# Performance work log

Measured on AMD Instinct MI355X. Metric: run time of the kernel, lower is better.

## Reference

```python
import jax, jax.numpy as jnp
import numpy as np

N_NODES = 100000
N_EDGES = 600000
IN_C, HID_C, OUT_C = 128, 128, 64


def gcn_conv(x, W, b, src, dst, n_nodes):
    """PyG GCNConv: out = D^{-1/2} (A + I) D^{-1/2} X W + b (symmetric norm, self-loops)."""
    h = x @ W  # [N, C_out] transform first (as PyG does)
    # add self loops
    loop = jnp.arange(n_nodes, dtype=src.dtype)
    s = jnp.concatenate([src, loop])
    d = jnp.concatenate([dst, loop])
    # degree over targets (edge weight = 1)
    deg = jax.ops.segment_sum(jnp.ones_like(d, dtype=h.dtype), d, num_segments=n_nodes)
    dinv = jnp.where(deg > 0, jax.lax.rsqrt(deg), 0.0)
    norm = dinv[s] * dinv[d]  # [E+N]
    msg = h[s] * norm[:, None]  # gather + scale
    out = jax.ops.segment_sum(msg, d, num_segments=n_nodes)  # scatter-add
    return out + b


def setup_inputs() -> dict:
    key = jax.random.key(0)
    k1, k2, k3, k4, k5 = jax.random.split(key, 5)
    x = jax.random.normal(k1, (N_NODES, IN_C), dtype=jnp.float32)
    src = jax.random.randint(k2, (N_EDGES,), 0, N_NODES, dtype=jnp.int32)
    dst = jax.random.randint(k3, (N_EDGES,), 0, N_NODES, dtype=jnp.int32)
    # Glorot-style init for conv weights, zero bias (PyG defaults)
    W1 = jax.random.normal(k4, (IN_C, HID_C), dtype=jnp.float32) * (1.0 / np.sqrt(IN_C))
    W2 = jax.random.normal(k5, (HID_C, OUT_C), dtype=jnp.float32) * (1.0 / np.sqrt(HID_C))
    b1 = jnp.zeros((HID_C,), dtype=jnp.float32)
    b2 = jnp.zeros((OUT_C,), dtype=jnp.float32)
    return {"x": x, "W1": W1, "b1": b1, "W2": W2, "b2": b2, "src": src, "dst": dst}


def reference(x, W1, b1, W2, b2, src, dst):
    h = gcn_conv(x, W1, b1, src, dst, N_NODES)
    h = jax.nn.relu(h)
    out = gcn_conv(h, W2, b2, src, dst, N_NODES)
    return out
```

## Files before the change

### kernel.cpp

```cpp
#include <hip/hip_runtime.h>
#include <math.h>


typedef __bf16 bf16x8 __attribute__((ext_vector_type(8)));
typedef float f32x4 __attribute__((ext_vector_type(4)));

union ABu {
  unsigned short u16[8];
  uint4 u4;
  bf16x8 v;
};

__device__ inline unsigned short f2bf(float f) {
  unsigned u = __float_as_uint(f);
  return (unsigned short)((u + 0x7fffu + ((u >> 16) & 1u)) >> 16);
}

__device__ inline void unpack8(uint4 v, float* f) {
  f[0] = __uint_as_float(v.x << 16);
  f[1] = __uint_as_float(v.x & 0xffff0000u);
  f[2] = __uint_as_float(v.y << 16);
  f[3] = __uint_as_float(v.y & 0xffff0000u);
  f[4] = __uint_as_float(v.z << 16);
  f[5] = __uint_as_float(v.z & 0xffff0000u);
  f[6] = __uint_as_float(v.w << 16);
  f[7] = __uint_as_float(v.w & 0xffff0000u);
}

__device__ inline uint4 pack8(const float* a) {
  uint4 o;
  o.x = (unsigned)f2bf(a[0]) | ((unsigned)f2bf(a[1]) << 16);
  o.y = (unsigned)f2bf(a[2]) | ((unsigned)f2bf(a[3]) << 16);
  o.z = (unsigned)f2bf(a[4]) | ((unsigned)f2bf(a[5]) << 16);
  o.w = (unsigned)f2bf(a[6]) | ((unsigned)f2bf(a[7]) << 16);
  return o;
}

constexpr int SCAN_CHUNK = 1024;

__global__ __launch_bounds__(256) void k_pre(const float* __restrict__ W1,
                                             const float* __restrict__ W2,
                                             unsigned short* __restrict__ Wb1,
                                             unsigned short* __restrict__ Wb2,
                                             int* __restrict__ counts, int n) {
  constexpr int CONV_BLOCKS = (128 * 128 + 128 * 64) / 256;
  if (blockIdx.x < CONV_BLOCKS) {
    int idx = blockIdx.x * 256 + threadIdx.x;
    if (idx < 128 * 128) {
      int k = idx >> 7, c = idx & 127;
      Wb1[(((k >> 3) << 7) + c) * 8 + (k & 7)] = f2bf(W1[idx]);
    } else {
      int j = idx - 128 * 128;
      int k = j >> 6, c = j & 63;
      Wb2[(((k >> 3) << 6) + c) * 8 + (k & 7)] = f2bf(W2[j]);
    }
    return;
  }
  int i = (blockIdx.x - CONV_BLOCKS) * 256 + threadIdx.x;
  if (i < n) counts[i] = 0;
}

__global__ __launch_bounds__(256) void k_gemm1(const float* __restrict__ X,
                                               const unsigned short* __restrict__ Wb,
                                               unsigned short* __restrict__ Cb, int M) {
  constexpr int K = 128, N = 128, NT = N / 16, KS = K / 32;
  const int tid = threadIdx.x;
  const int wave = tid >> 6;
  const int lane = tid & 63;
  const int q = lane >> 4;
  const int l15 = lane & 15;
  const int row0 = blockIdx.x * 64 + wave * 16;
  const int rowA = row0 + l15;

  f32x4 zero = {0.0f, 0.0f, 0.0f, 0.0f};
  f32x4 acc[NT];
#pragma unroll
  for (int t = 0; t < NT; ++t) acc[t] = zero;

#pragma unroll
  for (int kk = 0; kk < KS; ++kk) {
    ABu a;
    float4 f0 = make_float4(0.f, 0.f, 0.f, 0.f);
    float4 f1 = make_float4(0.f, 0.f, 0.f, 0.f);
    if (rowA < M) {
      const float4* ap = (const float4*)(X + (size_t)rowA * K + kk * 32 + q * 8);
      f0 = ap[0];
      f1 = ap[1];
    }
    a.u16[0] = f2bf(f0.x); a.u16[1] = f2bf(f0.y);
    a.u16[2] = f2bf(f0.z); a.u16[3] = f2bf(f0.w);
    a.u16[4] = f2bf(f1.x); a.u16[5] = f2bf(f1.y);
    a.u16[6] = f2bf(f1.z); a.u16[7] = f2bf(f1.w);
#pragma unroll
    for (int nt = 0; nt < NT; ++nt) {
      ABu b;
      b.u4 = *(const uint4*)(Wb + ((size_t)(kk * 4 + q) * N + nt * 16 + l15) * 8);
      acc[nt] = __builtin_amdgcn_mfma_f32_16x16x32_bf16(a.v, b.v, acc[nt], 0, 0, 0);
    }
  }

#pragma unroll
  for (int v = 0; v < 4; ++v) {
    int row = row0 + q * 4 + v;
    if (row < M) {
#pragma unroll
      for (int nt = 0; nt < NT; ++nt)
        Cb[(size_t)row * N + nt * 16 + l15] = f2bf(acc[nt][v]);
    }
  }
}

__global__ void k_count_rank(const int* __restrict__ dst, int* __restrict__ counts,
                             int* __restrict__ rank, int E) {
  int e = blockIdx.x * blockDim.x + threadIdx.x;
  if (e < E) rank[e] = atomicAdd(&counts[dst[e]], 1);
}

__global__ __launch_bounds__(256) void k_scan1(const int* __restrict__ counts,
                                               int* __restrict__ offsets,
                                               int* __restrict__ aux, int n) {
  __shared__ int tsum[256];
  int tid = threadIdx.x;
  int base = blockIdx.x * SCAN_CHUNK + tid * 4;
  int v0 = (base + 0 < n) ? counts[base + 0] : 0;
  int v1 = (base + 1 < n) ? counts[base + 1] : 0;
  int v2 = (base + 2 < n) ? counts[base + 2] : 0;
  int v3 = (base + 3 < n) ? counts[base + 3] : 0;
  int s = v0 + v1 + v2 + v3;
  tsum[tid] = s;
  __syncthreads();
  for (int off = 1; off < 256; off <<= 1) {
    int t = (tid >= off) ? tsum[tid - off] : 0;
    __syncthreads();
    tsum[tid] += t;
    __syncthreads();
  }
  int excl = tsum[tid] - s;
  if (base + 0 < n) offsets[base + 0] = excl;
  if (base + 1 < n) offsets[base + 1] = excl + v0;
  if (base + 2 < n) offsets[base + 2] = excl + v0 + v1;
  if (base + 3 < n) offsets[base + 3] = excl + v0 + v1 + v2;
  if (tid == 255) aux[blockIdx.x] = tsum[255];
}

__global__ __launch_bounds__(256) void k_scan3_dinv(int* __restrict__ offsets,
                                                    const int* __restrict__ aux,
                                                    const int* __restrict__ counts,
                                                    float* __restrict__ dinv,
                                                    int n, int E, int G) {
  __shared__ int saux[256];
  int tid = threadIdx.x;
  int v = (tid < G) ? aux[tid] : 0;
  saux[tid] = v;
  __syncthreads();
  for (int off = 1; off < 256; off <<= 1) {
    int t = (tid >= off) ? saux[tid - off] : 0;
    __syncthreads();
    saux[tid] += t;
    __syncthreads();
  }
  int excl = saux[tid] - v;
  __syncthreads();
  saux[tid] = excl;
  __syncthreads();

  int i = blockIdx.x * 256 + tid;
  if (i < n) {
    offsets[i] += saux[i >> 10];
    dinv[i] = rsqrtf((float)(counts[i] + 1));
  }
  if (i == 0) offsets[n] = E;
}

__global__ void k_scatter(const int* __restrict__ src, const int* __restrict__ dst,
                          const int* __restrict__ offsets, const int* __restrict__ rank,
                          int* __restrict__ esrc, int E) {
  int e = blockIdx.x * blockDim.x + threadIdx.x;
  if (e < E) esrc[offsets[dst[e]] + rank[e]] = src[e];
}

__global__ __launch_bounds__(256) void k_aggemm(const unsigned short* __restrict__ h1s,
                                                const float* __restrict__ dinv,
                                                const float* __restrict__ b1,
                                                const int* __restrict__ offsets,
                                                const int* __restrict__ esrc,
                                                const unsigned short* __restrict__ Wb2,
                                                unsigned short* __restrict__ h2s,
                                                int n) {
  constexpr int LDA = 136;
  __shared__ unsigned short As[16 * LDA];
  __shared__ float sdinv[16];
  const int tid = threadIdx.x;

  {
    const int nl = tid >> 4;
    const int q = tid & 15;
    const int node = blockIdx.x * 16 + nl;
    float acc[8];
    if (node < n) {
      const uint4* h4 = (const uint4*)h1s;
      float di = dinv[node];
      if (q == 0) sdinv[nl] = di;
      float hs[8];
      unpack8(h4[(size_t)node * 16 + q], hs);
#pragma unroll
      for (int i = 0; i < 8; ++i) acc[i] = hs[i] * di;
      int e0 = offsets[node];
      int e1 = offsets[node + 1];
      for (int e = e0; e < e1; e += 8) {
        int idx[8];
#pragma unroll
        for (int i = 0; i < 8; ++i) {
          int ee = e + i < e1 ? e + i : e1 - 1;
          idx[i] = esrc[ee];
        }
        uint4 rr[8];
        float dv[8];
#pragma unroll
        for (int i = 0; i < 8; ++i) {
          rr[i] = h4[(size_t)idx[i] * 16 + q];
          dv[i] = dinv[idx[i]];
        }
#pragma unroll
        for (int i = 0; i < 8; ++i) {
          float w = (e + i < e1) ? dv[i] : 0.f;
          float g[8];
          unpack8(rr[i], g);
#pragma unroll
          for (int j = 0; j < 8; ++j) acc[j] = fmaf(g[j], w, acc[j]);
        }
      }
      const float4* b14 = (const float4*)b1;
      float4 ba = b14[q * 2], bb = b14[q * 2 + 1];
      float bias[8] = {ba.x, ba.y, ba.z, ba.w, bb.x, bb.y, bb.z, bb.w};
#pragma unroll
      for (int i = 0; i < 8; ++i) acc[i] = fmaxf(fmaf(acc[i], di, bias[i]), 0.f);
    } else {
      if (q == 0) sdinv[nl] = 0.f;
#pragma unroll
      for (int i = 0; i < 8; ++i) acc[i] = 0.f;
    }
    *(uint4*)&As[nl * LDA + q * 8] = pack8(acc);
  }
  __syncthreads();

  {
    const int wave = tid >> 6;
    const int lane = tid & 63;
    const int q = lane >> 4;
    const int l15 = lane & 15;
    f32x4 acc = {0.0f, 0.0f, 0.0f, 0.0f};
#pragma unroll
    for (int kk = 0; kk < 4; ++kk) {
      ABu a, b;
      a.u4 = *(const uint4*)&As[l15 * LDA + kk * 32 + q * 8];
      b.u4 = *(const uint4*)(Wb2 + ((size_t)(kk * 4 + q) * 64 + wave * 16 + l15) * 8);
      acc = __builtin_amdgcn_mfma_f32_16x16x32_bf16(a.v, b.v, acc, 0, 0, 0);
    }
#pragma unroll
    for (int v = 0; v < 4; ++v) {
      int rl = q * 4 + v;
      int row = blockIdx.x * 16 + rl;
      if (row < n) h2s[(size_t)row * 64 + wave * 16 + l15] = f2bf(acc[v] * sdinv[rl]);
    }
  }
}

__global__ __launch_bounds__(256) void k_agg2(const unsigned short* __restrict__ h2s,
                                              const float* __restrict__ dinv,
                                              const float* __restrict__ b2,
                                              const int* __restrict__ offsets,
                                              const int* __restrict__ esrc,
                                              float* __restrict__ out, int n) {
  constexpr int CQ = 8;
  const int tid = threadIdx.x;
  const int node = blockIdx.x * 32 + tid / CQ;
  const int q = tid % CQ;
  if (node >= n) return;

  const uint4* h4 = (const uint4*)h2s;
  float di = dinv[node];
  float acc[8];
  unpack8(h4[(size_t)node * CQ + q], acc);

  int e0 = offsets[node];
  int e1 = offsets[node + 1];
  for (int e = e0; e < e1; e += 8) {
    int idx[8];
#pragma unroll
    for (int i = 0; i < 8; ++i) {
      int ee = e + i < e1 ? e + i : e1 - 1;
      idx[i] = esrc[ee];
    }
    uint4 rr[8];
#pragma unroll
    for (int i = 0; i < 8; ++i) rr[i] = h4[(size_t)idx[i] * CQ + q];
#pragma unroll
    for (int i = 0; i < 8; ++i) {
      float w = (e + i < e1) ? 1.f : 0.f;
      float g[8];
      unpack8(rr[i], g);
#pragma unroll
      for (int j = 0; j < 8; ++j) acc[j] = fmaf(g[j], w, acc[j]);
    }
  }

  const float4* b24 = (const float4*)b2;
  float4 ba = b24[q * 2], bb = b24[q * 2 + 1];
  float bias[8] = {ba.x, ba.y, ba.z, ba.w, bb.x, bb.y, bb.z, bb.w};
  float4 o0, o1;
  o0.x = fmaf(acc[0], di, bias[0]);
  o0.y = fmaf(acc[1], di, bias[1]);
  o0.z = fmaf(acc[2], di, bias[2]);
  o0.w = fmaf(acc[3], di, bias[3]);
  o1.x = fmaf(acc[4], di, bias[4]);
  o1.y = fmaf(acc[5], di, bias[5]);
  o1.z = fmaf(acc[6], di, bias[6]);
  o1.w = fmaf(acc[7], di, bias[7]);
  ((float4*)out)[(size_t)node * 16 + q * 2 + 0] = o0;
  ((float4*)out)[(size_t)node * 16 + q * 2 + 1] = o1;
}


extern "C" void kernel_launch(void* const* d_in, const int* in_sizes, int n_in,
                              void* d_out, int out_size, void* d_ws, size_t ws_size,
                              hipStream_t stream) {
  const float* x  = (const float*)d_in[0];
  const float* W1 = (const float*)d_in[1];
  const float* b1 = (const float*)d_in[2];
  const float* W2 = (const float*)d_in[3];
  const float* b2 = (const float*)d_in[4];
  const int* src  = (const int*)d_in[5];
  const int* dst  = (const int*)d_in[6];
  float* out = (float*)d_out;

  constexpr int IN_C = 128, HID_C = 128, OUT_C = 64;
  const int N = in_sizes[0] / IN_C;
  const int E = in_sizes[5];

  char* p = (char*)d_ws;
  auto alloc = [&](size_t bytes) {
    char* r = p;
    p += (bytes + 255) & ~(size_t)255;
    return r;
  };
  float* dinv    = (float*)alloc((size_t)N * 4);
  int*   offsets = (int*)alloc((size_t)(N + 1) * 4);
  int*   counts  = (int*)alloc((size_t)N * 4);
  int*   rank    = (int*)alloc((size_t)E * 4);
  int*   aux     = (int*)alloc(1024);
  int*   esrc    = (int*)alloc((size_t)E * 4);
  unsigned short* Wb1 = (unsigned short*)alloc((size_t)IN_C * HID_C * 2);
  unsigned short* Wb2 = (unsigned short*)alloc((size_t)HID_C * OUT_C * 2);
  unsigned short* h1s = (unsigned short*)alloc((size_t)N * HID_C * 2);
  unsigned short* h2s = (unsigned short*)alloc((size_t)N * OUT_C * 2);

  const int T = 256;
  const int G = (N + SCAN_CHUNK - 1) / SCAN_CHUNK;
  constexpr int CONV_BLOCKS = (128 * 128 + 128 * 64) / 256;

  k_pre<<<CONV_BLOCKS + (N + T - 1) / T, T, 0, stream>>>(W1, W2, Wb1, Wb2, counts, N);
  k_gemm1<<<(N + 63) / 64, T, 0, stream>>>(x, Wb1, h1s, N);
  k_count_rank<<<(E + T - 1) / T, T, 0, stream>>>(dst, counts, rank, E);
  k_scan1<<<G, T, 0, stream>>>(counts, offsets, aux, N);
  k_scan3_dinv<<<(N + T - 1) / T, T, 0, stream>>>(offsets, aux, counts, dinv, N, E, G);
  k_scatter<<<(E + T - 1) / T, T, 0, stream>>>(src, dst, offsets, rank, esrc, E);
  k_aggemm<<<(N + 15) / 16, T, 0, stream>>>(h1s, dinv, b1, offsets, esrc, Wb2, h2s, N);
  k_agg2<<<(N + 31) / 32, T, 0, stream>>>(h2s, dinv, b2, offsets, esrc, out, N);
}
```

Before: 214.1 us.

## Prescale GEMM1 output by dinv and vectorize edge preprocessing kernels

Moves the source-side dinv scaling into the first GEMM epilogue, so the layer-1 aggregation no longer gathers dinv for every neighbor. To make that possible, GEMM1 now runs after the degree and scan kernels, and dinv is computed in scan1 from the counts it already loaded. The count/rank and scatter kernels now handle four edges per thread using int4 loads. A side effect is that rounding of h1s to bf16 now happens after scaling, which slightly changes numerics.

```diff
diff --git a/kernel.cpp b/kernel.cpp
--- a/kernel.cpp
+++ b/kernel.cpp
@@ -60,8 +60,97 @@
   if (i < n) counts[i] = 0;
 }
 
+__global__ __launch_bounds__(256) void k_count_rank(const int* __restrict__ dst,
+                                                    int* __restrict__ counts,
+                                                    int* __restrict__ rank, int E) {
+  int base = (blockIdx.x * 256 + threadIdx.x) * 4;
+  if (base + 3 < E) {
+    int4 d = *(const int4*)(dst + base);
+    int4 r;
+    r.x = atomicAdd(&counts[d.x], 1);
+    r.y = atomicAdd(&counts[d.y], 1);
+    r.z = atomicAdd(&counts[d.z], 1);
+    r.w = atomicAdd(&counts[d.w], 1);
+    *(int4*)(rank + base) = r;
+  } else {
+    for (int e = base; e < E; ++e) rank[e] = atomicAdd(&counts[dst[e]], 1);
+  }
+}
+
+__global__ __launch_bounds__(256) void k_scan1(const int* __restrict__ counts,
+                                               int* __restrict__ offsets,
+                                               int* __restrict__ aux,
+                                               float* __restrict__ dinv, int n) {
+  __shared__ int tsum[256];
+  int tid = threadIdx.x;
+  int base = blockIdx.x * SCAN_CHUNK + tid * 4;
+  int v0 = (base + 0 < n) ? counts[base + 0] : 0;
+  int v1 = (base + 1 < n) ? counts[base + 1] : 0;
+  int v2 = (base + 2 < n) ? counts[base + 2] : 0;
+  int v3 = (base + 3 < n) ? counts[base + 3] : 0;
+  int s = v0 + v1 + v2 + v3;
+  tsum[tid] = s;
+  __syncthreads();
+  for (int off = 1; off < 256; off <<= 1) {
+    int t = (tid >= off) ? tsum[tid - off] : 0;
+    __syncthreads();
+    tsum[tid] += t;
+    __syncthreads();
+  }
+  int excl = tsum[tid] - s;
+  if (base + 0 < n) { offsets[base + 0] = excl;              dinv[base + 0] = rsqrtf((float)(v0 + 1)); }
+  if (base + 1 < n) { offsets[base + 1] = excl + v0;         dinv[base + 1] = rsqrtf((float)(v1 + 1)); }
+  if (base + 2 < n) { offsets[base + 2] = excl + v0 + v1;    dinv[base + 2] = rsqrtf((float)(v2 + 1)); }
+  if (base + 3 < n) { offsets[base + 3] = excl + v0 + v1 + v2; dinv[base + 3] = rsqrtf((float)(v3 + 1)); }
+  if (tid == 255) aux[blockIdx.x] = tsum[255];
+}
+
+__global__ __launch_bounds__(256) void k_scan3(int* __restrict__ offsets,
+                                               const int* __restrict__ aux,
+                                               int n, int E, int G) {
+  __shared__ int saux[256];
+  int tid = threadIdx.x;
+  int v = (tid < G) ? aux[tid] : 0;
+  saux[tid] = v;
+  __syncthreads();
+  for (int off = 1; off < 256; off <<= 1) {
+    int t = (tid >= off) ? saux[tid - off] : 0;
+    __syncthreads();
+    saux[tid] += t;
+    __syncthreads();
+  }
+  int excl = saux[tid] - v;
+  __syncthreads();
+  saux[tid] = excl;
+  __syncthreads();
+
+  int i = blockIdx.x * 256 + tid;
+  if (i < n) offsets[i] += saux[i >> 10];
+  if (i == 0) offsets[n] = E;
+}
+
+__global__ __launch_bounds__(256) void k_scatter(const int* __restrict__ src,
+                                                 const int* __restrict__ dst,
+                                                 const int* __restrict__ offsets,
+                                                 const int* __restrict__ rank,
+                                                 int* __restrict__ esrc, int E) {
+  int base = (blockIdx.x * 256 + threadIdx.x) * 4;
+  if (base + 3 < E) {
+    int4 s = *(const int4*)(src + base);
+    int4 d = *(const int4*)(dst + base);
+    int4 r = *(const int4*)(rank + base);
+    esrc[offsets[d.x] + r.x] = s.x;
+    esrc[offsets[d.y] + r.y] = s.y;
+    esrc[offsets[d.z] + r.z] = s.z;
+    esrc[offsets[d.w] + r.w] = s.w;
+  } else {
+    for (int e = base; e < E; ++e) esrc[offsets[dst[e]] + rank[e]] = src[e];
+  }
+}
+
 __global__ __launch_bounds__(256) void k_gemm1(const float* __restrict__ X,
                                                const unsigned short* __restrict__ Wb,
+                                               const float* __restrict__ dinv,
                                                unsigned short* __restrict__ Cb, int M) {
   constexpr int K = 128, N = 128, NT = N / 16, KS = K / 32;
   const int tid = threadIdx.x;
@@ -103,80 +192,12 @@
   for (int v = 0; v < 4; ++v) {
     int row = row0 + q * 4 + v;
     if (row < M) {
+      float di = dinv[row];
 #pragma unroll
       for (int nt = 0; nt < NT; ++nt)
-        Cb[(size_t)row * N + nt * 16 + l15] = f2bf(acc[nt][v]);
-    }
-  }
-}
-
-__global__ void k_count_rank(const int* __restrict__ dst, int* __restrict__ counts,
-                             int* __restrict__ rank, int E) {
-  int e = blockIdx.x * blockDim.x + threadIdx.x;
-  if (e < E) rank[e] = atomicAdd(&counts[dst[e]], 1);
-}
-
-__global__ __launch_bounds__(256) void k_scan1(const int* __restrict__ counts,
-                                               int* __restrict__ offsets,
-                                               int* __restrict__ aux, int n) {
-  __shared__ int tsum[256];
-  int tid = threadIdx.x;
-  int base = blockIdx.x * SCAN_CHUNK + tid * 4;
-  int v0 = (base + 0 < n) ? counts[base + 0] : 0;
-  int v1 = (base + 1 < n) ? counts[base + 1] : 0;
-  int v2 = (base + 2 < n) ? counts[base + 2] : 0;
-  int v3 = (base + 3 < n) ? counts[base + 3] : 0;
-  int s = v0 + v1 + v2 + v3;
-  tsum[tid] = s;
-  __syncthreads();
-  for (int off = 1; off < 256; off <<= 1) {
-    int t = (tid >= off) ? tsum[tid - off] : 0;
-    __syncthreads();
-    tsum[tid] += t;
-    __syncthreads();
-  }
-  int excl = tsum[tid] - s;
-  if (base + 0 < n) offsets[base + 0] = excl;
-  if (base + 1 < n) offsets[base + 1] = excl + v0;
-  if (base + 2 < n) offsets[base + 2] = excl + v0 + v1;
-  if (base + 3 < n) offsets[base + 3] = excl + v0 + v1 + v2;
-  if (tid == 255) aux[blockIdx.x] = tsum[255];
-}
-
-__global__ __launch_bounds__(256) void k_scan3_dinv(int* __restrict__ offsets,
-                                                    const int* __restrict__ aux,
-                                                    const int* __restrict__ counts,
-                                                    float* __restrict__ dinv,
-                                                    int n, int E, int G) {
-  __shared__ int saux[256];
-  int tid = threadIdx.x;
-  int v = (tid < G) ? aux[tid] : 0;
-  saux[tid] = v;
-  __syncthreads();
-  for (int off = 1; off < 256; off <<= 1) {
-    int t = (tid >= off) ? saux[tid - off] : 0;
-    __syncthreads();
-    saux[tid] += t;
-    __syncthreads();
-  }
-  int excl = saux[tid] - v;
-  __syncthreads();
-  saux[tid] = excl;
-  __syncthreads();
-
-  int i = blockIdx.x * 256 + tid;
-  if (i < n) {
-    offsets[i] += saux[i >> 10];
-    dinv[i] = rsqrtf((float)(counts[i] + 1));
-  }
-  if (i == 0) offsets[n] = E;
-}
-
-__global__ void k_scatter(const int* __restrict__ src, const int* __restrict__ dst,
-                          const int* __restrict__ offsets, const int* __restrict__ rank,
-                          int* __restrict__ esrc, int E) {
-  int e = blockIdx.x * blockDim.x + threadIdx.x;
-  if (e < E) esrc[offsets[dst[e]] + rank[e]] = src[e];
+        Cb[(size_t)row * N + nt * 16 + l15] = f2bf(acc[nt][v] * di);
+    }
+  }
 }
 
 __global__ __launch_bounds__(256) void k_aggemm(const unsigned short* __restrict__ h1s,
@@ -201,10 +222,7 @@
       const uint4* h4 = (const uint4*)h1s;
       float di = dinv[node];
       if (q == 0) sdinv[nl] = di;
-      float hs[8];
-      unpack8(h4[(size_t)node * 16 + q], hs);
-#pragma unroll
-      for (int i = 0; i < 8; ++i) acc[i] = hs[i] * di;
+      unpack8(h4[(size_t)node * 16 + q], acc);
       int e0 = offsets[node];
       int e1 = offsets[node + 1];
       for (int e = e0; e < e1; e += 8) {
@@ -215,15 +233,11 @@
           idx[i] = esrc[ee];
         }
         uint4 rr[8];
-        float dv[8];
+#pragma unroll
+        for (int i = 0; i < 8; ++i) rr[i] = h4[(size_t)idx[i] * 16 + q];
 #pragma unroll
         for (int i = 0; i < 8; ++i) {
-          rr[i] = h4[(size_t)idx[i] * 16 + q];
-          dv[i] = dinv[idx[i]];
-        }
-#pragma unroll
-        for (int i = 0; i < 8; ++i) {
-          float w = (e + i < e1) ? dv[i] : 0.f;
+          float w = (e + i < e1) ? 1.f : 0.f;
           float g[8];
           unpack8(rr[i], g);
 #pragma unroll
@@ -357,14 +371,15 @@
 
   const int T = 256;
   const int G = (N + SCAN_CHUNK - 1) / SCAN_CHUNK;
+  const int E4B = ((E + 3) / 4 + T - 1) / T;
   constexpr int CONV_BLOCKS = (128 * 128 + 128 * 64) / 256;
 
   k_pre<<<CONV_BLOCKS + (N + T - 1) / T, T, 0, stream>>>(W1, W2, Wb1, Wb2, counts, N);
-  k_gemm1<<<(N + 63) / 64, T, 0, stream>>>(x, Wb1, h1s, N);
-  k_count_rank<<<(E + T - 1) / T, T, 0, stream>>>(dst, counts, rank, E);
-  k_scan1<<<G, T, 0, stream>>>(counts, offsets, aux, N);
-  k_scan3_dinv<<<(N + T - 1) / T, T, 0, stream>>>(offsets, aux, counts, dinv, N, E, G);
-  k_scatter<<<(E + T - 1) / T, T, 0, stream>>>(src, dst, offsets, rank, esrc, E);
+  k_count_rank<<<E4B, T, 0, stream>>>(dst, counts, rank, E);
+  k_scan1<<<G, T, 0, stream>>>(counts, offsets, aux, dinv, N);
+  k_scan3<<<(N + T - 1) / T, T, 0, stream>>>(offsets, aux, N, E, G);
+  k_scatter<<<E4B, T, 0, stream>>>(src, dst, offsets, rank, esrc, E);
+  k_gemm1<<<(N + 63) / 64, T, 0, stream>>>(x, Wb1, dinv, h1s, N);
   k_aggemm<<<(N + 15) / 16, T, 0, stream>>>(h1s, dinv, b1, offsets, esrc, Wb2, h2s, N);
   k_agg2<<<(N + 31) / 32, T, 0, stream>>>(h2s, dinv, b2, offsets, esrc, out, N);
 }
```

After: 211.2 us. About the same (-1.4%).
